# Optimization experiments

Measured on AMD Instinct MI355X. Metric: run time of the kernel, lower is better.

The kernel has to match this reference:

```python
import jax, jax.numpy as jnp
import numpy as np

TEMPERATURE = 0.5  # sampler_config['temperature']
EPS = jnp.float32(np.finfo(np.float32).tiny)  # torch.finfo(float32).tiny


def setup_inputs() -> dict:
    key = jax.random.key(0)
    # att: [B graphs, N nodes per graph, M = Gnum_m subgraph samples]
    att = jax.random.normal(key, (256, 1024, 4), dtype=jnp.float32)
    return {"att": att, "k": 128}


def _continuous_topk(att, k, noise_key):
    """Iterative Gumbel-softmax relaxed top-k (Sampler.sample_subset +
    Sampler.continuous_topk with separate=False), batched over graphs (B)
    and subgraph samples (M).

    att: [B, N, M] node attention logits per graph per sample.
    Returns khot: [B, N, M], sum of k relaxed one-hot selections.
    """
    # gumbel_keys: z = -log(-log(U + eps))
    u = jax.random.uniform(noise_key, att.shape, dtype=att.dtype)
    att_g = att - jnp.log(-jnp.log(u + EPS))

    state0 = (att_g, jnp.zeros_like(att_g), jnp.zeros_like(att_g))

    def step(state, _):
        ag, onehot, khot = state
        khot_mask = jnp.maximum(1.0 - onehot, EPS)
        ag = ag + jnp.log(khot_mask)
        # softmax over the node axis (dim 0 of each per-graph slice in the original)
        onehot = jax.nn.softmax(ag / TEMPERATURE, axis=1)
        return (ag, onehot, khot + onehot), None

    (_, _, khot), _ = jax.lax.scan(step, state0, None, length=k)
    return khot


def reference(att, k):
    # Relaxed k-hot selection scores; the original then argsorts these per
    # graph to pick the top-k node indices (non-differentiable bookkeeping).
    return _continuous_topk(att, k, jax.random.key(42))
```

## Files before the change

kernel.cpp:

```cpp
#include <hip/hip_runtime.h>
#include <math.h>


#define N_NODES 1024
#define HEAD 4

typedef float f2 __attribute__((ext_vector_type(2)));

__device__ __forceinline__ unsigned rotl32(unsigned x, int r) {
  return (x << r) | (x >> (32 - r));
}

__device__ __forceinline__ void threefry2x32(unsigned k0, unsigned k1,
                                             unsigned& x0, unsigned& x1) {
  const unsigned ks0 = k0, ks1 = k1, ks2 = k0 ^ k1 ^ 0x1BD11BDAu;
  x0 += ks0; x1 += ks1;
  x0 += x1; x1 = rotl32(x1, 13); x1 ^= x0;
  x0 += x1; x1 = rotl32(x1, 15); x1 ^= x0;
  x0 += x1; x1 = rotl32(x1, 26); x1 ^= x0;
  x0 += x1; x1 = rotl32(x1, 6);  x1 ^= x0;
  x0 += ks1; x1 += ks2 + 1u;
  x0 += x1; x1 = rotl32(x1, 17); x1 ^= x0;
  x0 += x1; x1 = rotl32(x1, 29); x1 ^= x0;
  x0 += x1; x1 = rotl32(x1, 16); x1 ^= x0;
  x0 += x1; x1 = rotl32(x1, 24); x1 ^= x0;
  x0 += ks2; x1 += ks0 + 2u;
  x0 += x1; x1 = rotl32(x1, 13); x1 ^= x0;
  x0 += x1; x1 = rotl32(x1, 15); x1 ^= x0;
  x0 += x1; x1 = rotl32(x1, 26); x1 ^= x0;
  x0 += x1; x1 = rotl32(x1, 6);  x1 ^= x0;
  x0 += ks0; x1 += ks1 + 3u;
  x0 += x1; x1 = rotl32(x1, 17); x1 ^= x0;
  x0 += x1; x1 = rotl32(x1, 29); x1 ^= x0;
  x0 += x1; x1 = rotl32(x1, 16); x1 ^= x0;
  x0 += x1; x1 = rotl32(x1, 24); x1 ^= x0;
  x0 += ks1; x1 += ks2 + 4u;
  x0 += x1; x1 = rotl32(x1, 13); x1 ^= x0;
  x0 += x1; x1 = rotl32(x1, 15); x1 ^= x0;
  x0 += x1; x1 = rotl32(x1, 26); x1 ^= x0;
  x0 += x1; x1 = rotl32(x1, 6);  x1 ^= x0;
  x0 += ks2; x1 += ks0 + 5u;
}

template <int CTRL>
__device__ __forceinline__ float dpp_sum_step(float v) {
  int t = __builtin_amdgcn_update_dpp(0, __float_as_int(v), CTRL, 0xf, 0xf, true);
  return v + __int_as_float(t);
}
template <int CTRL>
__device__ __forceinline__ float dpp_max_step(float v) {
  int iv = __float_as_int(v);
  int t = __builtin_amdgcn_update_dpp(iv, iv, CTRL, 0xf, 0xf, false);
  return fmaxf(v, __int_as_float(t));
}

__device__ __forceinline__ float wave_sum64(float v) {
  v = dpp_sum_step<0x111>(v);
  v = dpp_sum_step<0x112>(v);
  v = dpp_sum_step<0x114>(v);
  v = dpp_sum_step<0x118>(v);
  v = dpp_sum_step<0x142>(v);
  v = dpp_sum_step<0x143>(v);
  return __int_as_float(__builtin_amdgcn_readlane(__float_as_int(v), 63));
}
__device__ __forceinline__ float wave_max64(float v) {
  v = dpp_max_step<0x111>(v);
  v = dpp_max_step<0x112>(v);
  v = dpp_max_step<0x114>(v);
  v = dpp_max_step<0x118>(v);
  v = dpp_max_step<0x142>(v);
  v = dpp_max_step<0x143>(v);
  return __int_as_float(__builtin_amdgcn_readlane(__float_as_int(v), 63));
}

__device__ __forceinline__ float lane_tree8(const f2* a) {
  f2 s0 = a[0] + a[1];
  f2 s1 = a[2] + a[3];
  f2 s2 = a[4] + a[5];
  f2 s3 = a[6] + a[7];
  f2 sA = s0 + s1;
  f2 sB = s2 + s3;
  f2 sC = sA + sB;
  return sC.x + sC.y;
}

__global__ __launch_bounds__(64, 1)
void Sampler_72619307040792_kernel(const float* __restrict__ att,
                                   const int* __restrict__ kp,
                                   float* __restrict__ out) {
  const int col = blockIdx.x;
  const int b = col >> 2;
  const int m = col & 3;
  const int lane = threadIdx.x;
  const int k = *kp;

  const float EPS = __uint_as_float(0x00800000u);
  const int base = b * 4096 + m;

  float g[16];
  f2 w[8], kh[8];

#pragma unroll
  for (int j = 0; j < 16; ++j) {
    const int n = j * 64 + lane;
    const unsigned idx = (unsigned)(base + n * 4);
    unsigned c0 = 0u, c1 = idx;
    threefry2x32(0u, 42u, c0, c1);
    const unsigned bits = c0 ^ c1;
    const float u = __uint_as_float((bits >> 9) | 0x3F800000u) - 1.0f;
    const float gum = -logf(-logf(u + EPS));
    g[j] = 2.0f * (att[idx] + gum);
  }

  float mx = g[0];
#pragma unroll
  for (int j = 1; j < 16; ++j) mx = fmaxf(mx, g[j]);
  mx = wave_max64(mx);

#pragma unroll
  for (int p = 0; p < 8; ++p) {
    f2 t;
    t.x = expf(g[2 * p] - mx);
    t.y = expf(g[2 * p + 1] - mx);
    w[p] = t;
    kh[p] = (f2)(0.0f);
  }

  const f2 one = (f2)(1.0f);
  float S, r;

  int it = 0;
  const int head = (k < HEAD) ? k : HEAD;
  for (; it < head; ++it) {
    S = wave_sum64(lane_tree8(w));
    r = __builtin_amdgcn_rcpf(S);
    f2 rv;
    rv.x = r;
    rv.y = r;
#pragma unroll
    for (int p = 0; p < 8; ++p)
      kh[p] = __builtin_elementwise_fma(w[p], rv, kh[p]);
#pragma unroll
    for (int p = 0; p < 8; ++p) {
      const f2 u = __builtin_elementwise_fma(-w[p], rv, one);
      const f2 t = w[p] * u;
      w[p] = t * u;
    }
  }

  if (it < k) {
    S = wave_sum64(lane_tree8(w));
    r = __builtin_amdgcn_rcpf(S);
    f2 w2[8];
#pragma unroll
    for (int p = 0; p < 8; ++p) w2[p] = w[p] * w[p];
    float tp = lane_tree8(w2);
    f2 qa = (f2)(0.0f), qb = (f2)(0.0f);
#pragma unroll
    for (int p = 0; p < 8; p += 2) {
      qa = __builtin_elementwise_fma(w2[p], w[p], qa);
      qb = __builtin_elementwise_fma(w2[p + 1], w[p + 1], qb);
    }
    {
      const f2 qs = qa + qb;
      float tq = qs.x + qs.y;

      for (; it < k; ++it) {
        const float P = wave_sum64(tp);
        const float Q = wave_sum64(tq);
        f2 rv;
        rv.x = r;
        rv.y = r;
#pragma unroll
        for (int p = 0; p < 8; ++p)
          kh[p] = __builtin_elementwise_fma(w[p], rv, kh[p]);
#pragma unroll
        for (int p = 0; p < 8; ++p) {
          const f2 u = __builtin_elementwise_fma(-w[p], rv, one);
          const f2 t = w[p] * u;
          w[p] = t * u;
        }
#pragma unroll
        for (int p = 0; p < 8; ++p) w2[p] = w[p] * w[p];
        tp = lane_tree8(w2);
        qa = (f2)(0.0f);
        qb = (f2)(0.0f);
#pragma unroll
        for (int p = 0; p < 8; p += 2) {
          qa = __builtin_elementwise_fma(w2[p], w[p], qa);
          qb = __builtin_elementwise_fma(w2[p + 1], w[p + 1], qb);
        }
        const f2 qs2 = qa + qb;
        tq = qs2.x + qs2.y;
        const float c1 = fmaf(-2.0f * r, P, S);
        S = fmaf(r * r, Q, c1);
        r = __builtin_amdgcn_rcpf(S);
      }
    }
  }

#pragma unroll
  for (int p = 0; p < 8; ++p) {
    out[base + (2 * p * 64 + lane) * 4] = kh[p].x;
    out[base + ((2 * p + 1) * 64 + lane) * 4] = kh[p].y;
  }
}

extern "C" void kernel_launch(void* const* d_in, const int* in_sizes, int n_in,
                              void* d_out, int out_size, void* d_ws, size_t ws_size,
                              hipStream_t stream) {
  const float* att = (const float*)d_in[0];
  const int* kp = (const int*)d_in[1];
  float* out = (float*)d_out;
  const int cols = out_size / N_NODES;
  Sampler_72619307040792_kernel<<<cols, 64, 0, stream>>>(att, kp, out);
}
```

Measured before the change: 39.19 us.

## Unroll relaxed top-k loop by two with fused S/P/Q wave reductions

Processes two softmax iterations per loop trip. S, P and Q are reduced with one interleaved DPP chain, and the second step's normalizer is predicted algebraically from them. This replaces the carried recurrence that needed two reductions per step. It aims to cut serialized cross-lane reductions per iteration and hide DPP latency through interleaving. It also adds an early exit for k<=0 and a remainder loop.

After: 31.69 us. 19.1% less time.

```diff
diff --git a/kernel.cpp b/kernel.cpp
--- a/kernel.cpp
+++ b/kernel.cpp
@@ -54,6 +54,10 @@
   return fmaxf(v, __int_as_float(t));
 }
 
+__device__ __forceinline__ float readlane63(float v) {
+  return __int_as_float(__builtin_amdgcn_readlane(__float_as_int(v), 63));
+}
+
 __device__ __forceinline__ float wave_sum64(float v) {
   v = dpp_sum_step<0x111>(v);
   v = dpp_sum_step<0x112>(v);
@@ -61,7 +65,7 @@
   v = dpp_sum_step<0x118>(v);
   v = dpp_sum_step<0x142>(v);
   v = dpp_sum_step<0x143>(v);
-  return __int_as_float(__builtin_amdgcn_readlane(__float_as_int(v), 63));
+  return readlane63(v);
 }
 __device__ __forceinline__ float wave_max64(float v) {
   v = dpp_max_step<0x111>(v);
@@ -70,7 +74,7 @@
   v = dpp_max_step<0x118>(v);
   v = dpp_max_step<0x142>(v);
   v = dpp_max_step<0x143>(v);
-  return __int_as_float(__builtin_amdgcn_readlane(__float_as_int(v), 63));
+  return readlane63(v);
 }
 
 __device__ __forceinline__ float lane_tree8(const f2* a) {
@@ -126,14 +130,22 @@
     kh[p] = (f2)(0.0f);
   }
 
+  if (k <= 0) {
+#pragma unroll
+    for (int p = 0; p < 8; ++p) {
+      out[base + (2 * p * 64 + lane) * 4] = 0.0f;
+      out[base + ((2 * p + 1) * 64 + lane) * 4] = 0.0f;
+    }
+    return;
+  }
+
   const f2 one = (f2)(1.0f);
-  float S, r;
-
   int it = 0;
+
   const int head = (k < HEAD) ? k : HEAD;
   for (; it < head; ++it) {
-    S = wave_sum64(lane_tree8(w));
-    r = __builtin_amdgcn_rcpf(S);
+    const float S = wave_sum64(lane_tree8(w));
+    const float r = __builtin_amdgcn_rcpf(S);
     f2 rv;
     rv.x = r;
     rv.y = r;
@@ -148,54 +160,88 @@
     }
   }
 
-  if (it < k) {
-    S = wave_sum64(lane_tree8(w));
-    r = __builtin_amdgcn_rcpf(S);
+  for (; it + 2 <= k; it += 2) {
     f2 w2[8];
 #pragma unroll
     for (int p = 0; p < 8; ++p) w2[p] = w[p] * w[p];
-    float tp = lane_tree8(w2);
+    const float sw = lane_tree8(w);
+    const float sp = lane_tree8(w2);
     f2 qa = (f2)(0.0f), qb = (f2)(0.0f);
 #pragma unroll
     for (int p = 0; p < 8; p += 2) {
       qa = __builtin_elementwise_fma(w2[p], w[p], qa);
       qb = __builtin_elementwise_fma(w2[p + 1], w[p + 1], qb);
     }
-    {
-      const f2 qs = qa + qb;
-      float tq = qs.x + qs.y;
-
-      for (; it < k; ++it) {
-        const float P = wave_sum64(tp);
-        const float Q = wave_sum64(tq);
-        f2 rv;
-        rv.x = r;
-        rv.y = r;
-#pragma unroll
-        for (int p = 0; p < 8; ++p)
-          kh[p] = __builtin_elementwise_fma(w[p], rv, kh[p]);
-#pragma unroll
-        for (int p = 0; p < 8; ++p) {
-          const f2 u = __builtin_elementwise_fma(-w[p], rv, one);
-          const f2 t = w[p] * u;
-          w[p] = t * u;
-        }
-#pragma unroll
-        for (int p = 0; p < 8; ++p) w2[p] = w[p] * w[p];
-        tp = lane_tree8(w2);
-        qa = (f2)(0.0f);
-        qb = (f2)(0.0f);
-#pragma unroll
-        for (int p = 0; p < 8; p += 2) {
-          qa = __builtin_elementwise_fma(w2[p], w[p], qa);
-          qb = __builtin_elementwise_fma(w2[p + 1], w[p + 1], qb);
-        }
-        const f2 qs2 = qa + qb;
-        tq = qs2.x + qs2.y;
-        const float c1 = fmaf(-2.0f * r, P, S);
-        S = fmaf(r * r, Q, c1);
-        r = __builtin_amdgcn_rcpf(S);
-      }
+    const f2 qs = qa + qb;
+    const float sq = qs.x + qs.y;
+
+    float vS = sw, vP = sp, vQ = sq;
+    vS = dpp_sum_step<0x111>(vS);
+    vP = dpp_sum_step<0x111>(vP);
+    vQ = dpp_sum_step<0x111>(vQ);
+    vS = dpp_sum_step<0x112>(vS);
+    vP = dpp_sum_step<0x112>(vP);
+    vQ = dpp_sum_step<0x112>(vQ);
+    vS = dpp_sum_step<0x114>(vS);
+    vP = dpp_sum_step<0x114>(vP);
+    vQ = dpp_sum_step<0x114>(vQ);
+    vS = dpp_sum_step<0x118>(vS);
+    vP = dpp_sum_step<0x118>(vP);
+    vQ = dpp_sum_step<0x118>(vQ);
+    vS = dpp_sum_step<0x142>(vS);
+    vP = dpp_sum_step<0x142>(vP);
+    vQ = dpp_sum_step<0x142>(vQ);
+    vS = dpp_sum_step<0x143>(vS);
+    vP = dpp_sum_step<0x143>(vP);
+    vQ = dpp_sum_step<0x143>(vQ);
+    const float S = readlane63(vS);
+    const float P = readlane63(vP);
+    const float Q = readlane63(vQ);
+
+    const float r = __builtin_amdgcn_rcpf(S);
+    const float S1 = fmaf(r * r, Q, fmaf(-2.0f * r, P, S));
+    const float r1 = __builtin_amdgcn_rcpf(S1);
+
+    f2 rv;
+    rv.x = r;
+    rv.y = r;
+#pragma unroll
+    for (int p = 0; p < 8; ++p)
+      kh[p] = __builtin_elementwise_fma(w[p], rv, kh[p]);
+#pragma unroll
+    for (int p = 0; p < 8; ++p) {
+      const f2 u = __builtin_elementwise_fma(-w[p], rv, one);
+      const f2 t = w[p] * u;
+      w[p] = t * u;
+    }
+    f2 rv1;
+    rv1.x = r1;
+    rv1.y = r1;
+#pragma unroll
+    for (int p = 0; p < 8; ++p)
+      kh[p] = __builtin_elementwise_fma(w[p], rv1, kh[p]);
+#pragma unroll
+    for (int p = 0; p < 8; ++p) {
+      const f2 u = __builtin_elementwise_fma(-w[p], rv1, one);
+      const f2 t = w[p] * u;
+      w[p] = t * u;
+    }
+  }
+
+  for (; it < k; ++it) {
+    const float S = wave_sum64(lane_tree8(w));
+    const float r = __builtin_amdgcn_rcpf(S);
+    f2 rv;
+    rv.x = r;
+    rv.y = r;
+#pragma unroll
+    for (int p = 0; p < 8; ++p)
+      kh[p] = __builtin_elementwise_fma(w[p], rv, kh[p]);
+#pragma unroll
+    for (int p = 0; p < 8; ++p) {
+      const f2 u = __builtin_elementwise_fma(-w[p], rv, one);
+      const f2 t = w[p] * u;
+      w[p] = t * u;
     }
   }
 
```
